# Kernel optimization log

Measured on AMD Instinct MI355X. Metric: run time of the kernel, lower is better.

## Reference

```python
import jax, jax.numpy as jnp
import numpy as np

N_NODES = 100000
N_EDGES = 3200000
N_FEAT = 512
HIDDEN = 16
N_CLASSES = 8


def setup_inputs() -> dict:
    key = jax.random.key(0)
    ks = jax.random.split(key, 7)
    x = jax.random.normal(ks[0], (N_NODES, N_FEAT), dtype=jnp.float32)
    edge_index = jax.random.randint(ks[1], (2, N_EDGES), 0, N_NODES, dtype=jnp.int64)
    # original code scales weights by /100; uniform weights are equivalent for testing
    edges_weight = jax.random.uniform(ks[2], (N_EDGES,), dtype=jnp.float32)
    # Glorot-ish params for the two GCNConv layers
    W1 = jax.random.normal(ks[3], (N_FEAT, HIDDEN), dtype=jnp.float32) / np.sqrt(N_FEAT)
    b1 = jnp.zeros((HIDDEN,), dtype=jnp.float32)
    W2 = jax.random.normal(ks[4], (HIDDEN, N_CLASSES), dtype=jnp.float32) / np.sqrt(HIDDEN)
    b2 = jnp.zeros((N_CLASSES,), dtype=jnp.float32)
    return {"x": x, "edge_index": edge_index, "edges_weight": edges_weight,
            "W1": W1, "b1": b1, "W2": W2, "b2": b2}


def _gcn_norm(edge_index, edges_weight, num_nodes):
    """PyG GCNConv normalization: add self-loops (weight 1), then
    norm_e = d^{-1/2}[src] * w_e * d^{-1/2}[dst] with d = weighted degree."""
    loop = jnp.arange(num_nodes, dtype=edge_index.dtype)
    src = jnp.concatenate([edge_index[0], loop])
    dst = jnp.concatenate([edge_index[1], loop])
    w = jnp.concatenate([edges_weight, jnp.ones((num_nodes,), edges_weight.dtype)])
    deg = jax.ops.segment_sum(w, dst, num_segments=num_nodes)
    dis = jnp.where(deg > 0, jax.lax.rsqrt(deg), 0.0)  # deg_inv_sqrt
    norm = dis[src] * w * dis[dst]
    return src, dst, norm


def _gcn_layer(h, W, b, src, dst, norm, num_nodes):
    h = h @ W                                 # transform first (small msg dim)
    msg = h[src] * norm[:, None]              # gather + edge scaling
    out = jax.ops.segment_sum(msg, dst, num_segments=num_nodes)  # scatter-add
    return out + b


def reference(x, edge_index, edges_weight, W1, b1, W2, b2):
    n = x.shape[0]
    src, dst, norm = _gcn_norm(edge_index, edges_weight, n)
    h = _gcn_layer(x, W1, b1, src, dst, norm, n)
    h = jax.nn.relu(h)
    h = _gcn_layer(h, W2, b2, src, dst, norm, n)
    return jax.nn.log_softmax(h, axis=1)
```

## Files before the change

### kernel.cpp

```cpp
#include <hip/hip_runtime.h>

#define TPB 256
constexpr int HID = 16;
constexpr int NC  = 8;

__device__ __forceinline__ void atomAddF(float* p, float v) {
    unsafeAtomicAdd(p, v);
}

__global__ void detect64_kernel(const int* __restrict__ ei, int E, int* flag) {
    int l = threadIdx.x;
    int v = 0;
    if (l < 32 && 2 * l + 1 < 2 * E) v = ei[2 * l + 1];
    unsigned long long b = __ballot(v != 0);
    if (l == 0) *flag = (b == 0ULL) ? 1 : 0;
}

__device__ __forceinline__ int edge_at(const int* __restrict__ ei, int index, int is64) {
    return is64 ? ei[2 * index] : ei[index];
}


__global__ void init_deg_kernel(float* deg, int N) {
    int i = blockIdx.x * TPB + threadIdx.x;
    if (i < N) deg[i] = 1.0f;
}

__global__ void init_nd_kernel(float* deg, int* cnt, int N) {
    int i = blockIdx.x * TPB + threadIdx.x;
    if (i < N) { deg[i] = 1.0f; cnt[i] = 0; }
}

__global__ void init_cnt_kernel(int* cnt, int N) {
    int i = blockIdx.x * TPB + threadIdx.x;
    if (i < N) cnt[i] = 0;
}

__global__ void dis_kernel(float* deg, int N) {
    int i = blockIdx.x * TPB + threadIdx.x;
    if (i < N) deg[i] = rsqrtf(deg[i]);
}

__global__ void gemm1_kernel(const float* __restrict__ x, const float* __restrict__ W,
                             float* __restrict__ h, int N, int K) {
    int row = blockIdx.x * TPB + threadIdx.x;
    if (row >= N) return;
    const float* xr = x + (size_t)row * K;
    float acc[HID];
#pragma unroll
    for (int j = 0; j < HID; ++j) acc[j] = 0.f;
    for (int k = 0; k < K; k += 4) {
        float4 xv = *reinterpret_cast<const float4*>(xr + k);
        const float* Wk = W + (size_t)k * HID;
#pragma unroll
        for (int kk = 0; kk < 4; ++kk) {
            float xs = (&xv.x)[kk];
#pragma unroll
            for (int j = 0; j < HID; ++j)
                acc[j] = fmaf(xs, Wk[kk * HID + j], acc[j]);
        }
    }
    float* hr = h + (size_t)row * HID;
#pragma unroll
    for (int j = 0; j < HID; j += 4)
        *reinterpret_cast<float4*>(hr + j) = make_float4(acc[j], acc[j+1], acc[j+2], acc[j+3]);
}

__global__ void gemm2_kernel(const float* __restrict__ agg1, const float* __restrict__ W2,
                             float* __restrict__ h2, int N) {
    int i = blockIdx.x * TPB + threadIdx.x;
    if (i >= N) return;
    const float* a = agg1 + (size_t)i * HID;
    float hv[HID];
#pragma unroll
    for (int k = 0; k < HID; k += 4) {
        float4 v = *reinterpret_cast<const float4*>(a + k);
        hv[k]     = fmaxf(v.x, 0.f);
        hv[k + 1] = fmaxf(v.y, 0.f);
        hv[k + 2] = fmaxf(v.z, 0.f);
        hv[k + 3] = fmaxf(v.w, 0.f);
    }
    float acc[NC];
#pragma unroll
    for (int c = 0; c < NC; ++c) acc[c] = 0.f;
#pragma unroll
    for (int k = 0; k < HID; ++k)
#pragma unroll
        for (int c = 0; c < NC; ++c)
            acc[c] = fmaf(hv[k], W2[k * NC + c], acc[c]);
    float* o = h2 + (size_t)i * NC;
    *reinterpret_cast<float4*>(o)     = make_float4(acc[0], acc[1], acc[2], acc[3]);
    *reinterpret_cast<float4*>(o + 4) = make_float4(acc[4], acc[5], acc[6], acc[7]);
}


__global__ void scatterP_kernel(const int* __restrict__ ei, const float* __restrict__ w,
                                int* __restrict__ cnt, uint2* __restrict__ edata,
                                int E, int C, const int* __restrict__ flag) {
    int e = blockIdx.x * TPB + threadIdx.x;
    if (e >= E) return;
    int is64 = *flag;
    int src = edge_at(ei, e, is64);
    int dst = edge_at(ei, E + e, is64);
    int pos = atomicAdd(&cnt[dst], 1);
    if (pos < C)
        edata[(size_t)dst * C + pos] = make_uint2((unsigned)src, __float_as_uint(w[e]));
}

__global__ void degP_kernel(const uint2* __restrict__ edata, const int* __restrict__ cnt,
                            float* __restrict__ dis, int N, int C) {
    int wid = (blockIdx.x * blockDim.x + threadIdx.x) >> 6;
    if (wid >= N) return;
    int lane = threadIdx.x & 63;
    int m = cnt[wid]; if (m > C) m = C;
    const uint2* seg = edata + (size_t)wid * C;
    float s = 0.f;
    for (int i = lane; i < m; i += 64) s += __uint_as_float(seg[i].y);
#pragma unroll
    for (int o = 1; o < 64; o <<= 1) s += __shfl_xor(s, o, 64);
    if (lane == 0) dis[wid] = rsqrtf(1.0f + s);
}

__global__ void agg1P_kernel(const uint2* __restrict__ edata, const int* __restrict__ cnt,
                             const float* __restrict__ h1, const float* __restrict__ dis,
                             const float* __restrict__ b1, float* __restrict__ agg1,
                             int N, int C) {
    int wid = (blockIdx.x * blockDim.x + threadIdx.x) >> 6;
    if (wid >= N) return;
    int lane = threadIdx.x & 63;
    int j = lane & 15, g = lane >> 4;
    int m = cnt[wid]; if (m > C) m = C;
    const uint2* seg = edata + (size_t)wid * C;
    float acc = 0.f;
    for (int i = g; i < m; i += 4) {
        uint2 u = seg[i];
        acc += dis[u.x] * __uint_as_float(u.y) * h1[(size_t)u.x * HID + j];
    }
    acc += __shfl_xor(acc, 16, 64);
    acc += __shfl_xor(acc, 32, 64);
    if (g == 0) {
        float dd = dis[wid];
        agg1[(size_t)wid * HID + j] = b1[j] + dd * (dd * h1[(size_t)wid * HID + j] + acc);
    }
}

__global__ void agg2P_lsm_kernel(const uint2* __restrict__ edata, const int* __restrict__ cnt,
                                 const float* __restrict__ h2, const float* __restrict__ dis,
                                 const float* __restrict__ b2, float* __restrict__ out,
                                 int N, int C) {
    int wid = (blockIdx.x * blockDim.x + threadIdx.x) >> 6;
    if (wid >= N) return;
    int lane = threadIdx.x & 63;
    int j = lane & 7, g = lane >> 3;
    int m = cnt[wid]; if (m > C) m = C;
    const uint2* seg = edata + (size_t)wid * C;
    float acc = 0.f;
    for (int i = g; i < m; i += 8) {
        uint2 u = seg[i];
        acc += dis[u.x] * __uint_as_float(u.y) * h2[(size_t)u.x * NC + j];
    }
    acc += __shfl_xor(acc, 8, 64);
    acc += __shfl_xor(acc, 16, 64);
    acc += __shfl_xor(acc, 32, 64);
    float dd = dis[wid];
    float v = b2[j] + dd * (dd * h2[(size_t)wid * NC + j] + acc);
    float mx = v;
    mx = fmaxf(mx, __shfl_xor(mx, 1, 64));
    mx = fmaxf(mx, __shfl_xor(mx, 2, 64));
    mx = fmaxf(mx, __shfl_xor(mx, 4, 64));
    float ex = expf(v - mx);
    float ssum = ex;
    ssum += __shfl_xor(ssum, 1, 64);
    ssum += __shfl_xor(ssum, 2, 64);
    ssum += __shfl_xor(ssum, 4, 64);
    float r = v - mx - logf(ssum);
    if (g == 0) out[(size_t)wid * NC + j] = r;
}


__global__ void hist_deg_kernel(const int* __restrict__ ei, const float* __restrict__ w,
                                int* __restrict__ cnt, float* __restrict__ deg,
                                int E, const int* __restrict__ flag) {
    int e = blockIdx.x * TPB + threadIdx.x;
    if (e >= E) return;
    int is64 = *flag;
    int dst = edge_at(ei, E + e, is64);
    atomicAdd(&cnt[dst], 1);
    atomAddF(&deg[dst], w[e]);
}

__global__ void scanA_kernel(const int* __restrict__ cnt, int* __restrict__ bsum, int N) {
    int i = blockIdx.x * 256 + threadIdx.x;
    int v = (i < N) ? cnt[i] : 0;
#pragma unroll
    for (int o = 32; o > 0; o >>= 1) v += __shfl_down(v, o, 64);
    __shared__ int ws[4];
    if ((threadIdx.x & 63) == 0) ws[threadIdx.x >> 6] = v;
    __syncthreads();
    if (threadIdx.x == 0) bsum[blockIdx.x] = ws[0] + ws[1] + ws[2] + ws[3];
}

__global__ void scanB_kernel(int* __restrict__ bsum, int NB, int* __restrict__ rowoffN, int E) {
    __shared__ int s[1024];
    int t = threadIdx.x;
    int v = (t < NB) ? bsum[t] : 0;
    s[t] = v;
    __syncthreads();
    for (int o = 1; o < 1024; o <<= 1) {
        int u = (t >= o) ? s[t - o] : 0;
        __syncthreads();
        s[t] += u;
        __syncthreads();
    }
    if (t < NB) bsum[t] = s[t] - v;
    if (t == 0) *rowoffN = E;
}

__global__ void scanC_kernel(const int* __restrict__ cnt, const int* __restrict__ bsum,
                             int* __restrict__ rowoff, int* __restrict__ cursor, int N) {
    __shared__ int s[256];
    int b = blockIdx.x, t = threadIdx.x;
    int i = b * 256 + t;
    int v = (i < N) ? cnt[i] : 0;
    s[t] = v;
    __syncthreads();
    for (int o = 1; o < 256; o <<= 1) {
        int u = (t >= o) ? s[t - o] : 0;
        __syncthreads();
        s[t] += u;
        __syncthreads();
    }
    if (i < N) {
        int ex = bsum[b] + s[t] - v;
        rowoff[i] = ex;
        cursor[i] = ex;
    }
}

__global__ void scatter_kernel(const int* __restrict__ ei, const float* __restrict__ w,
                               const float* __restrict__ dis, int* __restrict__ cursor,
                               int2* __restrict__ edata, int E, const int* __restrict__ flag) {
    int e = blockIdx.x * TPB + threadIdx.x;
    if (e >= E) return;
    int is64 = *flag;
    int src = edge_at(ei, e, is64);
    int dst = edge_at(ei, E + e, is64);
    float nrm = dis[src] * w[e] * dis[dst];
    int pos = atomicAdd(&cursor[dst], 1);
    edata[pos] = make_int2(src, __float_as_int(nrm));
}

__global__ void agg1_csr_kernel(const int2* __restrict__ edata, const int* __restrict__ rowoff,
                                const float* __restrict__ h1, const float* __restrict__ dis,
                                const float* __restrict__ b1, float* __restrict__ agg1, int N) {
    int wid = (blockIdx.x * blockDim.x + threadIdx.x) >> 6;
    if (wid >= N) return;
    int lane = threadIdx.x & 63;
    int j = lane & 15, g = lane >> 4;
    int s = rowoff[wid];
    int epd = rowoff[wid + 1] - s;
    float acc = 0.f;
    for (int i = g; i < epd; i += 4) {
        int2 d = edata[s + i];
        acc += __int_as_float(d.y) * h1[(size_t)d.x * HID + j];
    }
    acc += __shfl_xor(acc, 16, 64);
    acc += __shfl_xor(acc, 32, 64);
    if (g == 0) {
        float di = dis[wid];
        agg1[(size_t)wid * HID + j] = b1[j] + di * di * h1[(size_t)wid * HID + j] + acc;
    }
}

__global__ void agg2_lsm_kernel(const int2* __restrict__ edata, const int* __restrict__ rowoff,
                                const float* __restrict__ h2, const float* __restrict__ dis,
                                const float* __restrict__ b2, float* __restrict__ out, int N) {
    int wid = (blockIdx.x * blockDim.x + threadIdx.x) >> 6;
    if (wid >= N) return;
    int lane = threadIdx.x & 63;
    int j = lane & 7, g = lane >> 3;
    int s = rowoff[wid];
    int epd = rowoff[wid + 1] - s;
    float acc = 0.f;
    for (int i = g; i < epd; i += 8) {
        int2 d = edata[s + i];
        acc += __int_as_float(d.y) * h2[(size_t)d.x * NC + j];
    }
    acc += __shfl_xor(acc, 8, 64);
    acc += __shfl_xor(acc, 16, 64);
    acc += __shfl_xor(acc, 32, 64);
    float di = dis[wid];
    float v = b2[j] + di * di * h2[(size_t)wid * NC + j] + acc;
    float mx = v;
    mx = fmaxf(mx, __shfl_xor(mx, 1, 64));
    mx = fmaxf(mx, __shfl_xor(mx, 2, 64));
    mx = fmaxf(mx, __shfl_xor(mx, 4, 64));
    float ex = expf(v - mx);
    float ssum = ex;
    ssum += __shfl_xor(ssum, 1, 64);
    ssum += __shfl_xor(ssum, 2, 64);
    ssum += __shfl_xor(ssum, 4, 64);
    float r = v - mx - logf(ssum);
    if (g == 0) out[(size_t)wid * NC + j] = r;
}


__global__ void deg_edge_kernel(const int* __restrict__ ei, const float* __restrict__ w,
                                float* deg, int E, const int* __restrict__ flag) {
    int e = blockIdx.x * TPB + threadIdx.x;
    if (e >= E) return;
    int is64 = *flag;
    int dst = edge_at(ei, E + e, is64);
    atomAddF(&deg[dst], w[e]);
}

__global__ void init_agg1_kernel(const float* __restrict__ h1, const float* __restrict__ dis,
                                 const float* __restrict__ b1, float* __restrict__ agg1, int N) {
    int t = blockIdx.x * TPB + threadIdx.x;
    if (t >= N * HID) return;
    int i = t >> 4, j = t & 15;
    float d = dis[i];
    agg1[t] = b1[j] + d * d * h1[t];
}

__global__ void edge1_kernel(const int* __restrict__ ei, const float* __restrict__ w,
                             const float* __restrict__ dis, const float* __restrict__ h1,
                             float* __restrict__ agg1, int E, const int* __restrict__ flag) {
    int t = blockIdx.x * TPB + threadIdx.x;
    if (t >= E * HID) return;
    int e = t >> 4, j = t & 15;
    int is64 = *flag;
    int src = edge_at(ei, e, is64);
    int dst = edge_at(ei, E + e, is64);
    float nrm = dis[src] * w[e] * dis[dst];
    atomAddF(&agg1[dst * HID + j], nrm * h1[src * HID + j]);
}

__global__ void init_out_kernel(const float* __restrict__ h2, const float* __restrict__ dis,
                                const float* __restrict__ b2, float* __restrict__ out, int N) {
    int t = blockIdx.x * TPB + threadIdx.x;
    if (t >= N * NC) return;
    int i = t >> 3, j = t & 7;
    float d = dis[i];
    out[t] = b2[j] + d * d * h2[t];
}

__global__ void edge2_kernel(const int* __restrict__ ei, const float* __restrict__ w,
                             const float* __restrict__ dis, const float* __restrict__ h2,
                             float* __restrict__ out, int E, const int* __restrict__ flag) {
    int t = blockIdx.x * TPB + threadIdx.x;
    if (t >= E * NC) return;
    int e = t >> 3, j = t & 7;
    int is64 = *flag;
    int src = edge_at(ei, e, is64);
    int dst = edge_at(ei, E + e, is64);
    float nrm = dis[src] * w[e] * dis[dst];
    atomAddF(&out[dst * NC + j], nrm * h2[src * NC + j]);
}

__global__ void lsm_kernel(float* __restrict__ out, int N) {
    int i = blockIdx.x * TPB + threadIdx.x;
    if (i >= N) return;
    float* r = out + (size_t)i * NC;
    float4 a = *reinterpret_cast<const float4*>(r);
    float4 b = *reinterpret_cast<const float4*>(r + 4);
    float v[NC] = {a.x, a.y, a.z, a.w, b.x, b.y, b.z, b.w};
    float m = v[0];
#pragma unroll
    for (int j = 1; j < NC; ++j) m = fmaxf(m, v[j]);
    float s = 0.f;
#pragma unroll
    for (int j = 0; j < NC; ++j) s += expf(v[j] - m);
    float lse = m + logf(s);
#pragma unroll
    for (int j = 0; j < NC; ++j) v[j] -= lse;
    *reinterpret_cast<float4*>(r)     = make_float4(v[0], v[1], v[2], v[3]);
    *reinterpret_cast<float4*>(r + 4) = make_float4(v[4], v[5], v[6], v[7]);
}

extern "C" void kernel_launch(void* const* d_in, const int* in_sizes, int n_in,
                              void* d_out, int out_size, void* d_ws, size_t ws_size,
                              hipStream_t stream) {
    const float* x  = (const float*)d_in[0];
    const int*   ei = (const int*)d_in[1];
    const float* w  = (const float*)d_in[2];
    const float* W1 = (const float*)d_in[3];
    const float* b1 = (const float*)d_in[4];
    const float* W2 = (const float*)d_in[5];
    const float* b2 = (const float*)d_in[6];
    float* out = (float*)d_out;

    int E = in_sizes[2];
    int N = out_size / NC;
    int K = in_sizes[0] / N;

    auto nb = [](long long n) { return (int)((n + TPB - 1) / TPB); };
    int waveblocks = (int)(((long long)N * 64 + TPB - 1) / TPB);

    int C = 0;
    {
        int cands[3] = {96, 88, 80};
        for (int ci = 0; ci < 3; ++ci) {
            size_t need = (size_t)4 * ((size_t)2 * N * cands[ci] + (size_t)42 * N + 1);
            if (ws_size >= need) { C = cands[ci]; break; }
        }
    }

    if (C > 0) {
        uint2* edata = (uint2*)d_ws;
        float* h1    = (float*)(edata + (size_t)N * C);
        float* agg1  = h1 + (size_t)N * HID;
        float* h2    = agg1 + (size_t)N * HID;
        float* dis   = h2 + (size_t)N * NC;
        int*   cnt   = (int*)(dis + N);
        int*   flag  = cnt + N;

        detect64_kernel<<<1, 64, 0, stream>>>(ei, E, flag);
        init_cnt_kernel<<<nb(N), TPB, 0, stream>>>(cnt, N);
        gemm1_kernel<<<nb(N), TPB, 0, stream>>>(x, W1, h1, N, K);
        scatterP_kernel<<<nb(E), TPB, 0, stream>>>(ei, w, cnt, edata, E, C, flag);
        degP_kernel<<<waveblocks, TPB, 0, stream>>>(edata, cnt, dis, N, C);
        agg1P_kernel<<<waveblocks, TPB, 0, stream>>>(edata, cnt, h1, dis, b1, agg1, N, C);
        gemm2_kernel<<<nb(N), TPB, 0, stream>>>(agg1, W2, h2, N);
        agg2P_lsm_kernel<<<waveblocks, TPB, 0, stream>>>(edata, cnt, h2, dis, b2, out, N, C);
        return;
    }

    int NB = (N + 255) / 256;
    size_t need_csr = (size_t)4 * ((size_t)2 * E + (size_t)43 * N + 1026);
    bool use_csr = (ws_size >= need_csr) && (NB <= 1024);

    if (use_csr) {
        int2*  edata  = (int2*)d_ws;
        float* deg    = (float*)(edata + E);
        float* h1     = deg + N;
        float* agg1   = h1 + (size_t)N * HID;
        float* h2     = agg1 + (size_t)N * HID;
        int*   cnt    = (int*)(h2 + (size_t)N * NC);
        int*   rowoff = cnt + N;
        int*   cursor = rowoff + N + 1;
        int*   bsum   = cursor + N;
        int*   flag   = bsum + 1024;

        detect64_kernel<<<1, 64, 0, stream>>>(ei, E, flag);
        init_nd_kernel<<<nb(N), TPB, 0, stream>>>(deg, cnt, N);
        hist_deg_kernel<<<nb(E), TPB, 0, stream>>>(ei, w, cnt, deg, E, flag);
        dis_kernel<<<nb(N), TPB, 0, stream>>>(deg, N);
        scanA_kernel<<<NB, 256, 0, stream>>>(cnt, bsum, N);
        scanB_kernel<<<1, 1024, 0, stream>>>(bsum, NB, rowoff + N, E);
        scanC_kernel<<<NB, 256, 0, stream>>>(cnt, bsum, rowoff, cursor, N);
        gemm1_kernel<<<nb(N), TPB, 0, stream>>>(x, W1, h1, N, K);
        scatter_kernel<<<nb(E), TPB, 0, stream>>>(ei, w, deg, cursor, edata, E, flag);
        agg1_csr_kernel<<<waveblocks, TPB, 0, stream>>>(edata, rowoff, h1, deg, b1, agg1, N);
        gemm2_kernel<<<nb(N), TPB, 0, stream>>>(agg1, W2, h2, N);
        agg2_lsm_kernel<<<waveblocks, TPB, 0, stream>>>(edata, rowoff, h2, deg, b2, out, N);
    } else {
        float* deg  = (float*)d_ws;
        float* h1   = deg + N;
        float* agg1 = h1 + (size_t)N * HID;
        float* h2   = agg1 + (size_t)N * HID;
        int*   flag = (int*)(h2 + (size_t)N * NC);

        detect64_kernel<<<1, 64, 0, stream>>>(ei, E, flag);
        init_deg_kernel<<<nb(N), TPB, 0, stream>>>(deg, N);
        deg_edge_kernel<<<nb(E), TPB, 0, stream>>>(ei, w, deg, E, flag);
        dis_kernel<<<nb(N), TPB, 0, stream>>>(deg, N);
        gemm1_kernel<<<nb(N), TPB, 0, stream>>>(x, W1, h1, N, K);
        init_agg1_kernel<<<nb((long long)N * HID), TPB, 0, stream>>>(h1, deg, b1, agg1, N);
        edge1_kernel<<<nb((long long)E * HID), TPB, 0, stream>>>(ei, w, deg, h1, agg1, E, flag);
        gemm2_kernel<<<nb(N), TPB, 0, stream>>>(agg1, W2, h2, N);
        init_out_kernel<<<nb((long long)N * NC), TPB, 0, stream>>>(h2, deg, b2, out, N);
        edge2_kernel<<<nb((long long)E * NC), TPB, 0, stream>>>(ei, w, deg, h2, out, E, flag);
        lsm_kernel<<<nb(N), TPB, 0, stream>>>(out, N);
    }
}
```

Before: 748.7 us.

## Pre-scale node features by inverse sqrt degree and vectorize per-edge gathers in aggregation

The source-side d^{-1/2} factor is folded into the GEMM outputs (gemm1s/gemm2s run after the degree pass), which removes the per-edge gather of dis[src] from both aggregation kernels. The aggregation kernels now give one edge to each lane and load the whole 16- or 8-float feature row with float4 loads, then do a butterfly transpose-reduction across lanes. This trades the scattered 4-byte loads for wide row loads and fewer dis lookups, at the cost of more registers and more shuffles. The gemm1 launch moves after the degree pass, so it can no longer overlap with the scatter.

```diff
diff --git a/kernel.cpp b/kernel.cpp
--- a/kernel.cpp
+++ b/kernel.cpp
@@ -66,6 +66,34 @@
         *reinterpret_cast<float4*>(hr + j) = make_float4(acc[j], acc[j+1], acc[j+2], acc[j+3]);
 }
 
+__global__ void gemm1s_kernel(const float* __restrict__ x, const float* __restrict__ W,
+                              const float* __restrict__ dis, float* __restrict__ h, int N, int K) {
+    int row = blockIdx.x * TPB + threadIdx.x;
+    if (row >= N) return;
+    const float* xr = x + (size_t)row * K;
+    float acc[HID];
+#pragma unroll
+    for (int j = 0; j < HID; ++j) acc[j] = 0.f;
+    for (int k = 0; k < K; k += 4) {
+        float4 xv = *reinterpret_cast<const float4*>(xr + k);
+        const float* Wk = W + (size_t)k * HID;
+#pragma unroll
+        for (int kk = 0; kk < 4; ++kk) {
+            float xs = (&xv.x)[kk];
+#pragma unroll
+            for (int j = 0; j < HID; ++j)
+                acc[j] = fmaf(xs, Wk[kk * HID + j], acc[j]);
+        }
+    }
+    float d = dis[row];
+#pragma unroll
+    for (int j = 0; j < HID; ++j) acc[j] *= d;
+    float* hr = h + (size_t)row * HID;
+#pragma unroll
+    for (int j = 0; j < HID; j += 4)
+        *reinterpret_cast<float4*>(hr + j) = make_float4(acc[j], acc[j+1], acc[j+2], acc[j+3]);
+}
+
 __global__ void gemm2_kernel(const float* __restrict__ agg1, const float* __restrict__ W2,
                              float* __restrict__ h2, int N) {
     int i = blockIdx.x * TPB + threadIdx.x;
@@ -88,6 +116,36 @@
 #pragma unroll
         for (int c = 0; c < NC; ++c)
             acc[c] = fmaf(hv[k], W2[k * NC + c], acc[c]);
+    float* o = h2 + (size_t)i * NC;
+    *reinterpret_cast<float4*>(o)     = make_float4(acc[0], acc[1], acc[2], acc[3]);
+    *reinterpret_cast<float4*>(o + 4) = make_float4(acc[4], acc[5], acc[6], acc[7]);
+}
+
+__global__ void gemm2s_kernel(const float* __restrict__ agg1, const float* __restrict__ W2,
+                              const float* __restrict__ dis, float* __restrict__ h2, int N) {
+    int i = blockIdx.x * TPB + threadIdx.x;
+    if (i >= N) return;
+    const float* a = agg1 + (size_t)i * HID;
+    float hv[HID];
+#pragma unroll
+    for (int k = 0; k < HID; k += 4) {
+        float4 v = *reinterpret_cast<const float4*>(a + k);
+        hv[k]     = fmaxf(v.x, 0.f);
+        hv[k + 1] = fmaxf(v.y, 0.f);
+        hv[k + 2] = fmaxf(v.z, 0.f);
+        hv[k + 3] = fmaxf(v.w, 0.f);
+    }
+    float acc[NC];
+#pragma unroll
+    for (int c = 0; c < NC; ++c) acc[c] = 0.f;
+#pragma unroll
+    for (int k = 0; k < HID; ++k)
+#pragma unroll
+        for (int c = 0; c < NC; ++c)
+            acc[c] = fmaf(hv[k], W2[k * NC + c], acc[c]);
+    float d = dis[i];
+#pragma unroll
+    for (int c = 0; c < NC; ++c) acc[c] *= d;
     float* o = h2 + (size_t)i * NC;
     *reinterpret_cast<float4*>(o)     = make_float4(acc[0], acc[1], acc[2], acc[3]);
     *reinterpret_cast<float4*>(o + 4) = make_float4(acc[4], acc[5], acc[6], acc[7]);
@@ -102,9 +160,10 @@
     int is64 = *flag;
     int src = edge_at(ei, e, is64);
     int dst = edge_at(ei, E + e, is64);
+    float wv = w[e];
     int pos = atomicAdd(&cnt[dst], 1);
     if (pos < C)
-        edata[(size_t)dst * C + pos] = make_uint2((unsigned)src, __float_as_uint(w[e]));
+        edata[(size_t)dst * C + pos] = make_uint2((unsigned)src, __float_as_uint(wv));
 }
 
 __global__ void degP_kernel(const uint2* __restrict__ edata, const int* __restrict__ cnt,
@@ -122,48 +181,118 @@
 }
 
 __global__ void agg1P_kernel(const uint2* __restrict__ edata, const int* __restrict__ cnt,
-                             const float* __restrict__ h1, const float* __restrict__ dis,
+                             const float* __restrict__ h1s, const float* __restrict__ dis,
                              const float* __restrict__ b1, float* __restrict__ agg1,
                              int N, int C) {
     int wid = (blockIdx.x * blockDim.x + threadIdx.x) >> 6;
     if (wid >= N) return;
     int lane = threadIdx.x & 63;
-    int j = lane & 15, g = lane >> 4;
     int m = cnt[wid]; if (m > C) m = C;
     const uint2* seg = edata + (size_t)wid * C;
-    float acc = 0.f;
-    for (int i = g; i < m; i += 4) {
+    float acc[HID];
+#pragma unroll
+    for (int j = 0; j < HID; ++j) acc[j] = 0.f;
+    for (int i = lane; i < m; i += 64) {
         uint2 u = seg[i];
-        acc += dis[u.x] * __uint_as_float(u.y) * h1[(size_t)u.x * HID + j];
-    }
-    acc += __shfl_xor(acc, 16, 64);
-    acc += __shfl_xor(acc, 32, 64);
-    if (g == 0) {
+        float wv = __uint_as_float(u.y);
+        const float* hr = h1s + (size_t)u.x * HID;
+        float4 a = *reinterpret_cast<const float4*>(hr);
+        float4 b = *reinterpret_cast<const float4*>(hr + 4);
+        float4 c = *reinterpret_cast<const float4*>(hr + 8);
+        float4 d = *reinterpret_cast<const float4*>(hr + 12);
+        acc[0]  = fmaf(wv, a.x, acc[0]);  acc[1]  = fmaf(wv, a.y, acc[1]);
+        acc[2]  = fmaf(wv, a.z, acc[2]);  acc[3]  = fmaf(wv, a.w, acc[3]);
+        acc[4]  = fmaf(wv, b.x, acc[4]);  acc[5]  = fmaf(wv, b.y, acc[5]);
+        acc[6]  = fmaf(wv, b.z, acc[6]);  acc[7]  = fmaf(wv, b.w, acc[7]);
+        acc[8]  = fmaf(wv, c.x, acc[8]);  acc[9]  = fmaf(wv, c.y, acc[9]);
+        acc[10] = fmaf(wv, c.z, acc[10]); acc[11] = fmaf(wv, c.w, acc[11]);
+        acc[12] = fmaf(wv, d.x, acc[12]); acc[13] = fmaf(wv, d.y, acc[13]);
+        acc[14] = fmaf(wv, d.z, acc[14]); acc[15] = fmaf(wv, d.w, acc[15]);
+    }
+#pragma unroll
+    for (int j = 0; j < HID; ++j) {
+        acc[j] += __shfl_xor(acc[j], 16, 64);
+        acc[j] += __shfl_xor(acc[j], 32, 64);
+    }
+#pragma unroll
+    for (int t = 0; t < 8; ++t) {
+        float lo = __shfl_xor(acc[t], 8, 64);
+        float hi = __shfl_xor(acc[t + 8], 8, 64);
+        acc[t] = (lane & 8) ? (acc[t + 8] + hi) : (acc[t] + lo);
+    }
+#pragma unroll
+    for (int t = 0; t < 4; ++t) {
+        float lo = __shfl_xor(acc[t], 4, 64);
+        float hi = __shfl_xor(acc[t + 4], 4, 64);
+        acc[t] = (lane & 4) ? (acc[t + 4] + hi) : (acc[t] + lo);
+    }
+#pragma unroll
+    for (int t = 0; t < 2; ++t) {
+        float lo = __shfl_xor(acc[t], 2, 64);
+        float hi = __shfl_xor(acc[t + 2], 2, 64);
+        acc[t] = (lane & 2) ? (acc[t + 2] + hi) : (acc[t] + lo);
+    }
+    {
+        float lo = __shfl_xor(acc[0], 1, 64);
+        float hi = __shfl_xor(acc[1], 1, 64);
+        acc[0] = (lane & 1) ? (acc[1] + hi) : (acc[0] + lo);
+    }
+    if (lane < HID) {
         float dd = dis[wid];
-        agg1[(size_t)wid * HID + j] = b1[j] + dd * (dd * h1[(size_t)wid * HID + j] + acc);
+        agg1[(size_t)wid * HID + lane] =
+            b1[lane] + dd * (h1s[(size_t)wid * HID + lane] + acc[0]);
     }
 }
 
 __global__ void agg2P_lsm_kernel(const uint2* __restrict__ edata, const int* __restrict__ cnt,
-                                 const float* __restrict__ h2, const float* __restrict__ dis,
+                                 const float* __restrict__ h2s, const float* __restrict__ dis,
                                  const float* __restrict__ b2, float* __restrict__ out,
                                  int N, int C) {
     int wid = (blockIdx.x * blockDim.x + threadIdx.x) >> 6;
     if (wid >= N) return;
     int lane = threadIdx.x & 63;
-    int j = lane & 7, g = lane >> 3;
     int m = cnt[wid]; if (m > C) m = C;
     const uint2* seg = edata + (size_t)wid * C;
-    float acc = 0.f;
-    for (int i = g; i < m; i += 8) {
+    float acc[NC];
+#pragma unroll
+    for (int j = 0; j < NC; ++j) acc[j] = 0.f;
+    for (int i = lane; i < m; i += 64) {
         uint2 u = seg[i];
-        acc += dis[u.x] * __uint_as_float(u.y) * h2[(size_t)u.x * NC + j];
-    }
-    acc += __shfl_xor(acc, 8, 64);
-    acc += __shfl_xor(acc, 16, 64);
-    acc += __shfl_xor(acc, 32, 64);
+        float wv = __uint_as_float(u.y);
+        const float* hr = h2s + (size_t)u.x * NC;
+        float4 a = *reinterpret_cast<const float4*>(hr);
+        float4 b = *reinterpret_cast<const float4*>(hr + 4);
+        acc[0] = fmaf(wv, a.x, acc[0]);  acc[1] = fmaf(wv, a.y, acc[1]);
+        acc[2] = fmaf(wv, a.z, acc[2]);  acc[3] = fmaf(wv, a.w, acc[3]);
+        acc[4] = fmaf(wv, b.x, acc[4]);  acc[5] = fmaf(wv, b.y, acc[5]);
+        acc[6] = fmaf(wv, b.z, acc[6]);  acc[7] = fmaf(wv, b.w, acc[7]);
+    }
+#pragma unroll
+    for (int j = 0; j < NC; ++j) {
+        acc[j] += __shfl_xor(acc[j], 8, 64);
+        acc[j] += __shfl_xor(acc[j], 16, 64);
+        acc[j] += __shfl_xor(acc[j], 32, 64);
+    }
+#pragma unroll
+    for (int t = 0; t < 4; ++t) {
+        float lo = __shfl_xor(acc[t], 4, 64);
+        float hi = __shfl_xor(acc[t + 4], 4, 64);
+        acc[t] = (lane & 4) ? (acc[t + 4] + hi) : (acc[t] + lo);
+    }
+#pragma unroll
+    for (int t = 0; t < 2; ++t) {
+        float lo = __shfl_xor(acc[t], 2, 64);
+        float hi = __shfl_xor(acc[t + 2], 2, 64);
+        acc[t] = (lane & 2) ? (acc[t + 2] + hi) : (acc[t] + lo);
+    }
+    {
+        float lo = __shfl_xor(acc[0], 1, 64);
+        float hi = __shfl_xor(acc[1], 1, 64);
+        acc[0] = (lane & 1) ? (acc[1] + hi) : (acc[0] + lo);
+    }
+    int c = lane & 7;
     float dd = dis[wid];
-    float v = b2[j] + dd * (dd * h2[(size_t)wid * NC + j] + acc);
+    float v = b2[c] + dd * (h2s[(size_t)wid * NC + c] + acc[0]);
     float mx = v;
     mx = fmaxf(mx, __shfl_xor(mx, 1, 64));
     mx = fmaxf(mx, __shfl_xor(mx, 2, 64));
@@ -174,7 +303,7 @@
     ssum += __shfl_xor(ssum, 2, 64);
     ssum += __shfl_xor(ssum, 4, 64);
     float r = v - mx - logf(ssum);
-    if (g == 0) out[(size_t)wid * NC + j] = r;
+    if (lane < NC) out[(size_t)wid * NC + lane] = r;
 }
 
 
@@ -408,21 +537,21 @@
 
     if (C > 0) {
         uint2* edata = (uint2*)d_ws;
-        float* h1    = (float*)(edata + (size_t)N * C);
-        float* agg1  = h1 + (size_t)N * HID;
-        float* h2    = agg1 + (size_t)N * HID;
-        float* dis   = h2 + (size_t)N * NC;
+        float* h1s   = (float*)(edata + (size_t)N * C);
+        float* agg1  = h1s + (size_t)N * HID;
+        float* h2s   = agg1 + (size_t)N * HID;
+        float* dis   = h2s + (size_t)N * NC;
         int*   cnt   = (int*)(dis + N);
         int*   flag  = cnt + N;
 
         detect64_kernel<<<1, 64, 0, stream>>>(ei, E, flag);
         init_cnt_kernel<<<nb(N), TPB, 0, stream>>>(cnt, N);
-        gemm1_kernel<<<nb(N), TPB, 0, stream>>>(x, W1, h1, N, K);
         scatterP_kernel<<<nb(E), TPB, 0, stream>>>(ei, w, cnt, edata, E, C, flag);
         degP_kernel<<<waveblocks, TPB, 0, stream>>>(edata, cnt, dis, N, C);
-        agg1P_kernel<<<waveblocks, TPB, 0, stream>>>(edata, cnt, h1, dis, b1, agg1, N, C);
-        gemm2_kernel<<<nb(N), TPB, 0, stream>>>(agg1, W2, h2, N);
-        agg2P_lsm_kernel<<<waveblocks, TPB, 0, stream>>>(edata, cnt, h2, dis, b2, out, N, C);
+        gemm1s_kernel<<<nb(N), TPB, 0, stream>>>(x, W1, dis, h1s, N, K);
+        agg1P_kernel<<<waveblocks, TPB, 0, stream>>>(edata, cnt, h1s, dis, b1, agg1, N, C);
+        gemm2s_kernel<<<nb(N), TPB, 0, stream>>>(agg1, W2, dis, h2s, N);
+        agg2P_lsm_kernel<<<waveblocks, TPB, 0, stream>>>(edata, cnt, h2s, dis, b2, out, N, C);
         return;
     }
 
```

New measurement: 722.4 us. -3.5%, faster.
